# Kernel optimization log

Measured on AMD Instinct MI355X. Metric: run time of the kernel, lower is better.

The kernel has to match this reference:

```python
import jax, jax.numpy as jnp
import numpy as np

B, P, N, E = 4, 4, 4096, 512
QKV_DIM, HEADS = 512, 8
DH = QKV_DIM // HEADS
EPS = 1e-12  # F.normalize default eps


def setup_inputs() -> dict:
    key = jax.random.key(0)
    ks = jax.random.split(key, 5)
    s = 1.0 / np.sqrt(E)
    return {
        "x": jax.random.normal(ks[0], (B, P, N, E), dtype=jnp.float32),
        "w_qkv": jax.random.normal(ks[1], (3 * QKV_DIM, E), dtype=jnp.float32) * s,
        "b_qkv": jax.random.normal(ks[2], (3 * QKV_DIM,), dtype=jnp.float32) * 0.01,
        "temperature": jnp.ones((HEADS, 1, 1), dtype=jnp.float32),
        "w_out": jax.random.normal(ks[3], (E, QKV_DIM), dtype=jnp.float32) * (1.0 / np.sqrt(QKV_DIM)),
        "b_out": jax.random.normal(ks[4], (E,), dtype=jnp.float32) * 0.01,
    }


def _l2norm(t):
    # F.normalize(t, dim=-1): t / max(||t||_2, eps)
    n = jnp.sqrt(jnp.sum(t * t, axis=-1, keepdims=True))
    return t / jnp.maximum(n, EPS)


def reference(x, w_qkv, b_qkv, temperature, w_out, b_out):
    b, p, n, _ = x.shape
    qkv = x @ w_qkv.T + b_qkv                      # (b,p,n,3*qkv)
    q, k, v = jnp.split(qkv, 3, axis=-1)
    def to_heads(t):
        # (b,p,n,h*dh) -> (b,p,h,dh,n)  (channels-as-tokens)
        t = t.reshape(b, p, n, HEADS, DH)
        return jnp.transpose(t, (0, 1, 3, 4, 2))
    q, k, v = to_heads(q), to_heads(k), to_heads(v)
    q = _l2norm(q)                                  # normalize over tokens n
    k = _l2norm(k)
    # channel-wise (dh x dh) attention per head, temperature-scaled
    attn = jnp.einsum('bphdn,bphen->bphde', q, k) * temperature  # (b,p,h,dh,dh)
    attn = jax.nn.softmax(attn, axis=-1)
    out = jnp.einsum('bphde,bphen->bphdn', attn, v)               # (b,p,h,dh,n)
    # torch rearrange 'b p h n d -> b p d (h n)' on (b,p,h,dh,n) -> (b,p,n,h*dh)
    out = jnp.transpose(out, (0, 1, 4, 2, 3)).reshape(b, p, n, HEADS * DH)
    return out @ w_out.T + b_out
```

## Files before the change

kernel.cpp:

```cpp
#include <hip/hip_runtime.h>
#include <stdint.h>

typedef unsigned short u16;
typedef __bf16 bf16x8 __attribute__((ext_vector_type(8)));
typedef float f32x4 __attribute__((ext_vector_type(4)));

#define AS1 __attribute__((address_space(1)))
#define AS3 __attribute__((address_space(3)))

__device__ __forceinline__ void gload_lds16(u16* lds_wave_base, const u16* g) {
  __builtin_amdgcn_global_load_lds((AS1 void*)g, (AS3 void*)lds_wave_base, 16, 0, 0);
}

__device__ __forceinline__ u16 f2bf(float f) {
  unsigned int u = __float_as_uint(f);
  u += 0x7fffu + ((u >> 16) & 1u);
  return (u16)(u >> 16);
}

__global__ void cast_f32_bf16(const float* __restrict__ in, u16* __restrict__ out, int n8) {
  int i = blockIdx.x * blockDim.x + threadIdx.x;
  if (i >= n8) return;
  const float4* p = (const float4*)in + (size_t)i * 2;
  float4 a = p[0], b = p[1];
  uint2 lo, hi;
  lo.x = (unsigned)f2bf(a.x) | ((unsigned)f2bf(a.y) << 16);
  lo.y = (unsigned)f2bf(a.z) | ((unsigned)f2bf(a.w) << 16);
  hi.x = (unsigned)f2bf(b.x) | ((unsigned)f2bf(b.y) << 16);
  hi.y = (unsigned)f2bf(b.z) | ((unsigned)f2bf(b.w) << 16);
  uint2* o = (uint2*)out + (size_t)i * 2;
  o[0] = lo;
  o[1] = hi;
}

template <int MODE>
__global__ __launch_bounds__(256) void gemm_bt(const u16* __restrict__ gA,
                                               const u16* __restrict__ gB,
                                               const float* __restrict__ bias,
                                               void* __restrict__ gC) {
  __shared__ __align__(16) u16 As[128 * 32];
  __shared__ __align__(16) u16 Bs[128 * 32];
  const int t = threadIdx.x;
  const int w = t >> 6, l = t & 63;
  const int lrow = l & 15, quad = l >> 4;
  const int wm = (w >> 1) * 64, wn = (w & 1) * 64;
  const int m0 = blockIdx.x * 128, n0 = blockIdx.y * 128;
  if (MODE == 2) {
    gA += (size_t)blockIdx.z * (512 * 512);
    gB += (size_t)blockIdx.z * (4096 * 512);
  }
  const int srow = w * 32 + (l >> 2);
  const int scol = (l & 3) * 8;
  const u16* ga0 = gA + (size_t)(m0 + srow) * 512 + scol;
  const u16* ga1 = gA + (size_t)(m0 + srow + 16) * 512 + scol;
  const u16* gb0 = gB + (size_t)(n0 + srow) * 512 + scol;
  const u16* gb1 = gB + (size_t)(n0 + srow + 16) * 512 + scol;
  u16* lA0 = &As[w * 1024];
  u16* lA1 = &As[w * 1024 + 512];
  u16* lB0 = &Bs[w * 1024];
  u16* lB1 = &Bs[w * 1024 + 512];

  f32x4 acc[4][4];
#pragma unroll
  for (int mi = 0; mi < 4; ++mi)
#pragma unroll
    for (int ni = 0; ni < 4; ++ni) acc[mi][ni] = (f32x4){0.f, 0.f, 0.f, 0.f};

#pragma unroll 1
  for (int k0 = 0; k0 < 512; k0 += 32) {
    gload_lds16(lA0, ga0 + k0);
    gload_lds16(lA1, ga1 + k0);
    gload_lds16(lB0, gb0 + k0);
    gload_lds16(lB1, gb1 + k0);
    __syncthreads();
    bf16x8 af[4], bfr[4];
#pragma unroll
    for (int mi = 0; mi < 4; ++mi)
      af[mi] = *(const bf16x8*)&As[(wm + mi * 16 + lrow) * 32 + quad * 8];
#pragma unroll
    for (int ni = 0; ni < 4; ++ni)
      bfr[ni] = *(const bf16x8*)&Bs[(wn + ni * 16 + lrow) * 32 + quad * 8];
#pragma unroll
    for (int mi = 0; mi < 4; ++mi)
#pragma unroll
      for (int ni = 0; ni < 4; ++ni)
        acc[mi][ni] = __builtin_amdgcn_mfma_f32_16x16x32_bf16(af[mi], bfr[ni], acc[mi][ni], 0, 0, 0);
    __syncthreads();
  }

#pragma unroll
  for (int mi = 0; mi < 4; ++mi) {
    const int mrow = m0 + wm + mi * 16 + quad * 4;
#pragma unroll
    for (int ni = 0; ni < 4; ++ni) {
      const int ncol = n0 + wn + ni * 16 + lrow;
      f32x4 v = acc[mi][ni];
      if (MODE == 0) {
        const int bp = mrow >> 12, n = mrow & 4095;
        const float bb = bias[ncol];
        uint2 pk;
        pk.x = (unsigned)f2bf(v[0] + bb) | ((unsigned)f2bf(v[1] + bb) << 16);
        pk.y = (unsigned)f2bf(v[2] + bb) | ((unsigned)f2bf(v[3] + bb) << 16);
        *(uint2*)((u16*)gC + (((size_t)bp << 22) + ((size_t)ncol << 12) + n)) = pk;
      } else if (MODE == 1) {
        const int bp = ncol >> 12, n = ncol & 4095;
        const float4 bb = *(const float4*)&bias[1024 + mrow];
        uint2 pk;
        pk.x = (unsigned)f2bf(v[0] + bb.x) | ((unsigned)f2bf(v[1] + bb.y) << 16);
        pk.y = (unsigned)f2bf(v[2] + bb.z) | ((unsigned)f2bf(v[3] + bb.w) << 16);
        *(uint2*)((u16*)gC + ((size_t)bp * (4096 * 512) + (size_t)n * 512 + mrow)) = pk;
      } else {
        const float4 bb = *(const float4*)&bias[mrow];
        float4 o;
        o.x = v[0] + bb.x;
        o.y = v[1] + bb.y;
        o.z = v[2] + bb.z;
        o.w = v[3] + bb.w;
        *(float4*)((float*)gC + (((size_t)blockIdx.z * 4096 + ncol) * 512 + mrow)) = o;
      }
    }
  }
}

__global__ __launch_bounds__(512) void attn_weff(const u16* __restrict__ QKt,
                                                 const u16* __restrict__ wout,
                                                 const float* __restrict__ temperature,
                                                 u16* __restrict__ Weff) {
  __shared__ __align__(16) float sattn[64 * 64];
  __shared__ __align__(16) u16 sattnT[64 * 64];
  __shared__ float rn[128];
  const int blk = blockIdx.x;
  const int bp = blk >> 3, h = blk & 7;
  const int t = threadIdx.x, w = t >> 6, l = t & 63;
  const int lrow = l & 15, quad = l >> 4;
  const u16* base = QKt + ((size_t)bp << 22);

  for (int i = t; i < 4096; i += 512) sattn[i] = 0.f;

#pragma unroll 1
  for (int rr = 0; rr < 16; ++rr) {
    const int i = w * 16 + rr;
    const int ch = (i < 64) ? (h * 64 + i) : (448 + h * 64 + i);
    const u16* row = base + ((size_t)ch << 12);
    float s = 0.f;
#pragma unroll
    for (int it = 0; it < 8; ++it) {
      bf16x8 a = *(const bf16x8*)(row + (it * 64 + l) * 8);
#pragma unroll
      for (int j = 0; j < 8; ++j) {
        float vv = (float)a[j];
        s += vv * vv;
      }
    }
#pragma unroll
    for (int off = 1; off < 64; off <<= 1) s += __shfl_xor(s, off);
    if (l == 0) rn[i] = 1.f / fmaxf(sqrtf(s), 1e-12f);
  }

  f32x4 acc[4][4];
#pragma unroll
  for (int mi = 0; mi < 4; ++mi)
#pragma unroll
    for (int ni = 0; ni < 4; ++ni) acc[mi][ni] = (f32x4){0.f, 0.f, 0.f, 0.f};
  const u16* qb = base + ((size_t)(h * 64) << 12);
  const u16* kb = base + ((size_t)(512 + h * 64) << 12);
  const int nbase = w * 512;
#pragma unroll 1
  for (int ks = 0; ks < 16; ++ks) {
    const int nn = nbase + ks * 32 + quad * 8;
    bf16x8 af[4], bfr[4];
#pragma unroll
    for (int mi = 0; mi < 4; ++mi)
      af[mi] = *(const bf16x8*)(qb + (((size_t)(mi * 16 + lrow)) << 12) + nn);
#pragma unroll
    for (int ni = 0; ni < 4; ++ni)
      bfr[ni] = *(const bf16x8*)(kb + (((size_t)(ni * 16 + lrow)) << 12) + nn);
#pragma unroll
    for (int mi = 0; mi < 4; ++mi)
#pragma unroll
      for (int ni = 0; ni < 4; ++ni)
        acc[mi][ni] = __builtin_amdgcn_mfma_f32_16x16x32_bf16(af[mi], bfr[ni], acc[mi][ni], 0, 0, 0);
  }
  __syncthreads();
  for (int ww = 0; ww < 8; ++ww) {
    if (w == ww) {
#pragma unroll
      for (int mi = 0; mi < 4; ++mi)
#pragma unroll
        for (int ni = 0; ni < 4; ++ni)
#pragma unroll
          for (int r = 0; r < 4; ++r)
            sattn[(mi * 16 + quad * 4 + r) * 64 + ni * 16 + lrow] += acc[mi][ni][r];
    }
    __syncthreads();
  }

  if (t < 64) {
    const int d = t;
    const float rq = rn[d];
    const float tmp = temperature[h];
    float mx = -1e30f;
    for (int e = 0; e < 64; ++e) {
      const int idx = (e + d) & 63;
      float v = sattn[d * 64 + idx] * rq * rn[64 + idx] * tmp;
      sattn[d * 64 + idx] = v;
      mx = fmaxf(mx, v);
    }
    float s = 0.f;
    for (int e = 0; e < 64; ++e) {
      const int idx = (e + d) & 63;
      float p = __expf(sattn[d * 64 + idx] - mx);
      s += p;
      sattn[d * 64 + idx] = p;
    }
    const float inv = 1.f / s;
    for (int e = 0; e < 64; ++e) sattnT[e * 64 + d] = f2bf(sattn[d * 64 + e] * inv);
  }
  __syncthreads();

  bf16x8 a0[4], a1[4];
#pragma unroll
  for (int mi = 0; mi < 4; ++mi) {
    a0[mi] = *(const bf16x8*)&sattnT[(mi * 16 + lrow) * 64 + quad * 8];
    a1[mi] = *(const bf16x8*)&sattnT[(mi * 16 + lrow) * 64 + 32 + quad * 8];
  }
  u16* wb = Weff + ((size_t)bp * (512 * 512));
#pragma unroll 1
  for (int nb = 0; nb < 4; ++nb) {
    const int co = (w * 4 + nb) * 16 + lrow;
    const u16* wrow = wout + (size_t)co * 512 + h * 64;
    bf16x8 b0 = *(const bf16x8*)(wrow + quad * 8);
    bf16x8 b1 = *(const bf16x8*)(wrow + 32 + quad * 8);
#pragma unroll
    for (int mi = 0; mi < 4; ++mi) {
      f32x4 c = (f32x4){0.f, 0.f, 0.f, 0.f};
      c = __builtin_amdgcn_mfma_f32_16x16x32_bf16(a0[mi], b0, c, 0, 0, 0);
      c = __builtin_amdgcn_mfma_f32_16x16x32_bf16(a1[mi], b1, c, 0, 0, 0);
      const int e0 = mi * 16 + quad * 4;
      uint2 pk;
      pk.x = (unsigned)f2bf(c[0]) | ((unsigned)f2bf(c[1]) << 16);
      pk.y = (unsigned)f2bf(c[2]) | ((unsigned)f2bf(c[3]) << 16);
      *(uint2*)(wb + (size_t)co * 512 + h * 64 + e0) = pk;
    }
  }
}

extern "C" void kernel_launch(void* const* d_in, const int* in_sizes, int n_in,
                              void* d_out, int out_size, void* d_ws, size_t ws_size,
                              hipStream_t stream) {
  const float* x      = (const float*)d_in[0];
  const float* w_qkv  = (const float*)d_in[1];
  const float* b_qkv  = (const float*)d_in[2];
  const float* temp   = (const float*)d_in[3];
  const float* w_out  = (const float*)d_in[4];
  const float* b_out  = (const float*)d_in[5];
  float* y = (float*)d_out;

  char* ws = (char*)d_ws;
  u16* x_bf    = (u16*)(ws);
  u16* wqkv_bf = (u16*)(ws + 67108864);
  u16* wout_bf = (u16*)(ws + 68681728);
  u16* QKt     = (u16*)(ws + 69206016);
  u16* V_nat   = (u16*)(ws + 203423744);
  u16* Weff    = (u16*)(ws + 270532608);

  cast_f32_bf16<<<16384, 256, 0, stream>>>(x, x_bf, 33554432 / 8);
  cast_f32_bf16<<<384, 256, 0, stream>>>(w_qkv, wqkv_bf, 786432 / 8);
  cast_f32_bf16<<<128, 256, 0, stream>>>(w_out, wout_bf, 262144 / 8);

  gemm_bt<0><<<dim3(512, 8), 256, 0, stream>>>(x_bf, wqkv_bf, b_qkv, QKt);
  gemm_bt<1><<<dim3(4, 512), 256, 0, stream>>>(wqkv_bf + 1024 * 512, x_bf, b_qkv, V_nat);
  attn_weff<<<128, 512, 0, stream>>>(QKt, wout_bf, temp, Weff);
  gemm_bt<2><<<dim3(4, 32, 16), 256, 0, stream>>>(Weff, V_nat, b_out, y);
}
```

Baseline: 591.0 us.

## Stage GEMM epilogue through LDS and fuse Q/K norm sums into QKV GEMM

The MODE 0/1 GEMM epilogues now transpose the output tile through padded LDS and write coalesced 16-byte rows, replacing the scattered 8-byte stores. The QKV GEMM also accumulates per-channel sums of squares and adds them into a workspace buffer with atomics, so attn_weff no longer rereads the whole Q/K tensor to compute L2 norms. Grid order for MODE 0 is swapped so adjacent blocks walk along tokens. This adds a memset, float atomics whose order is nondeterministic, and norms taken from fp32 values rather than the rounded bf16 ones.

```diff
diff --git a/kernel.cpp b/kernel.cpp
--- a/kernel.cpp
+++ b/kernel.cpp
@@ -37,24 +37,30 @@
 __global__ __launch_bounds__(256) void gemm_bt(const u16* __restrict__ gA,
                                                const u16* __restrict__ gB,
                                                const float* __restrict__ bias,
-                                               void* __restrict__ gC) {
-  __shared__ __align__(16) u16 As[128 * 32];
-  __shared__ __align__(16) u16 Bs[128 * 32];
+                                               void* __restrict__ gC,
+                                               float* __restrict__ ssq) {
+  constexpr int SMEM_U16 = (MODE == 2) ? 8192 : (128 * 136);
+  __shared__ __align__(16) u16 smem[SMEM_U16];
+  u16* As = smem;
+  u16* Bs = smem + 4096;
   const int t = threadIdx.x;
   const int w = t >> 6, l = t & 63;
   const int lrow = l & 15, quad = l >> 4;
   const int wm = (w >> 1) * 64, wn = (w & 1) * 64;
-  const int m0 = blockIdx.x * 128, n0 = blockIdx.y * 128;
+  const int m0 = (MODE == 0 ? blockIdx.y : blockIdx.x) * 128;
+  const int n0 = (MODE == 0 ? blockIdx.x : blockIdx.y) * 128;
+  const u16* pA = gA;
+  const u16* pB = gB;
   if (MODE == 2) {
-    gA += (size_t)blockIdx.z * (512 * 512);
-    gB += (size_t)blockIdx.z * (4096 * 512);
+    pA += (size_t)blockIdx.z * (512 * 512);
+    pB += (size_t)blockIdx.z * (4096 * 512);
   }
   const int srow = w * 32 + (l >> 2);
   const int scol = (l & 3) * 8;
-  const u16* ga0 = gA + (size_t)(m0 + srow) * 512 + scol;
-  const u16* ga1 = gA + (size_t)(m0 + srow + 16) * 512 + scol;
-  const u16* gb0 = gB + (size_t)(n0 + srow) * 512 + scol;
-  const u16* gb1 = gB + (size_t)(n0 + srow + 16) * 512 + scol;
+  const u16* ga0 = pA + (size_t)(m0 + srow) * 512 + scol;
+  const u16* ga1 = pA + (size_t)(m0 + srow + 16) * 512 + scol;
+  const u16* gb0 = pB + (size_t)(n0 + srow) * 512 + scol;
+  const u16* gb1 = pB + (size_t)(n0 + srow + 16) * 512 + scol;
   u16* lA0 = &As[w * 1024];
   u16* lA1 = &As[w * 1024 + 512];
   u16* lB0 = &Bs[w * 1024];
@@ -88,29 +94,15 @@
     __syncthreads();
   }
 
-#pragma unroll
-  for (int mi = 0; mi < 4; ++mi) {
-    const int mrow = m0 + wm + mi * 16 + quad * 4;
-#pragma unroll
-    for (int ni = 0; ni < 4; ++ni) {
-      const int ncol = n0 + wn + ni * 16 + lrow;
-      f32x4 v = acc[mi][ni];
-      if (MODE == 0) {
-        const int bp = mrow >> 12, n = mrow & 4095;
-        const float bb = bias[ncol];
-        uint2 pk;
-        pk.x = (unsigned)f2bf(v[0] + bb) | ((unsigned)f2bf(v[1] + bb) << 16);
-        pk.y = (unsigned)f2bf(v[2] + bb) | ((unsigned)f2bf(v[3] + bb) << 16);
-        *(uint2*)((u16*)gC + (((size_t)bp << 22) + ((size_t)ncol << 12) + n)) = pk;
-      } else if (MODE == 1) {
-        const int bp = ncol >> 12, n = ncol & 4095;
-        const float4 bb = *(const float4*)&bias[1024 + mrow];
-        uint2 pk;
-        pk.x = (unsigned)f2bf(v[0] + bb.x) | ((unsigned)f2bf(v[1] + bb.y) << 16);
-        pk.y = (unsigned)f2bf(v[2] + bb.z) | ((unsigned)f2bf(v[3] + bb.w) << 16);
-        *(uint2*)((u16*)gC + ((size_t)bp * (4096 * 512) + (size_t)n * 512 + mrow)) = pk;
-      } else {
-        const float4 bb = *(const float4*)&bias[mrow];
+  if (MODE == 2) {
+#pragma unroll
+    for (int mi = 0; mi < 4; ++mi) {
+      const int mrow = m0 + wm + mi * 16 + quad * 4;
+      const float4 bb = *(const float4*)&bias[mrow];
+#pragma unroll
+      for (int ni = 0; ni < 4; ++ni) {
+        const int ncol = n0 + wn + ni * 16 + lrow;
+        f32x4 v = acc[mi][ni];
         float4 o;
         o.x = v[0] + bb.x;
         o.y = v[1] + bb.y;
@@ -119,12 +111,70 @@
         *(float4*)((float*)gC + (((size_t)blockIdx.z * 4096 + ncol) * 512 + mrow)) = o;
       }
     }
+  } else {
+    float ss[4] = {0.f, 0.f, 0.f, 0.f};
+#pragma unroll
+    for (int mi = 0; mi < 4; ++mi) {
+      const int mrow_l = wm + mi * 16 + quad * 4;
+#pragma unroll
+      for (int ni = 0; ni < 4; ++ni) {
+        const int ncol_l = wn + ni * 16 + lrow;
+        f32x4 v = acc[mi][ni];
+        float f0, f1, f2, f3;
+        if (MODE == 0) {
+          const float bb = bias[n0 + ncol_l];
+          f0 = v[0] + bb;
+          f1 = v[1] + bb;
+          f2 = v[2] + bb;
+          f3 = v[3] + bb;
+          ss[ni] += f0 * f0 + f1 * f1 + f2 * f2 + f3 * f3;
+        } else {
+          const float4 bb = *(const float4*)&bias[1024 + m0 + mrow_l];
+          f0 = v[0] + bb.x;
+          f1 = v[1] + bb.y;
+          f2 = v[2] + bb.z;
+          f3 = v[3] + bb.w;
+        }
+        uint2 pk;
+        pk.x = (unsigned)f2bf(f0) | ((unsigned)f2bf(f1) << 16);
+        pk.y = (unsigned)f2bf(f2) | ((unsigned)f2bf(f3) << 16);
+        *(uint2*)&smem[ncol_l * 136 + mrow_l] = pk;
+      }
+    }
+    if (MODE == 0) {
+#pragma unroll
+      for (int ni = 0; ni < 4; ++ni) {
+        float s = ss[ni];
+        s += __shfl_xor(s, 16);
+        s += __shfl_xor(s, 32);
+        if (quad == 0)
+          atomicAdd(&ssq[((m0 >> 12) << 10) + n0 + wn + ni * 16 + lrow], s);
+      }
+    }
+    __syncthreads();
+    u16* outp = (u16*)gC;
+#pragma unroll
+    for (int j = 0; j < 8; ++j) {
+      const int g = j * 256 + t;
+      const int r = g >> 4;
+      const int c = (g & 15) * 8;
+      uint4 val = *(const uint4*)&smem[r * 136 + c];
+      size_t gaddr;
+      if (MODE == 0) {
+        gaddr = ((size_t)(m0 >> 12) << 22) + ((size_t)(n0 + r) << 12) + (size_t)((m0 & 4095) + c);
+      } else {
+        const int tokg = n0 + r;
+        gaddr = (size_t)(tokg >> 12) * (4096 * 512) + (size_t)(tokg & 4095) * 512 + (size_t)(m0 + c);
+      }
+      *(uint4*)(outp + gaddr) = val;
+    }
   }
 }
 
 __global__ __launch_bounds__(512) void attn_weff(const u16* __restrict__ QKt,
                                                  const u16* __restrict__ wout,
                                                  const float* __restrict__ temperature,
+                                                 const float* __restrict__ ssq,
                                                  u16* __restrict__ Weff) {
   __shared__ __align__(16) float sattn[64 * 64];
   __shared__ __align__(16) u16 sattnT[64 * 64];
@@ -137,24 +187,10 @@
 
   for (int i = t; i < 4096; i += 512) sattn[i] = 0.f;
 
-#pragma unroll 1
-  for (int rr = 0; rr < 16; ++rr) {
-    const int i = w * 16 + rr;
-    const int ch = (i < 64) ? (h * 64 + i) : (448 + h * 64 + i);
-    const u16* row = base + ((size_t)ch << 12);
-    float s = 0.f;
-#pragma unroll
-    for (int it = 0; it < 8; ++it) {
-      bf16x8 a = *(const bf16x8*)(row + (it * 64 + l) * 8);
-#pragma unroll
-      for (int j = 0; j < 8; ++j) {
-        float vv = (float)a[j];
-        s += vv * vv;
-      }
-    }
-#pragma unroll
-    for (int off = 1; off < 64; off <<= 1) s += __shfl_xor(s, off);
-    if (l == 0) rn[i] = 1.f / fmaxf(sqrtf(s), 1e-12f);
+  if (t < 128) {
+    const int ch = (t < 64) ? (h * 64 + t) : (448 + h * 64 + t);
+    const float nn = sqrtf(ssq[(bp << 10) + ch]);
+    rn[t] = 1.f / fmaxf(nn, 1e-12f);
   }
 
   f32x4 acc[4][4];
@@ -263,13 +299,15 @@
   u16* QKt     = (u16*)(ws + 69206016);
   u16* V_nat   = (u16*)(ws + 203423744);
   u16* Weff    = (u16*)(ws + 270532608);
-
+  float* ssq   = (float*)(ws + 278921216);
+
+  hipMemsetAsync(ssq, 0, 16 * 1024 * sizeof(float), stream);
   cast_f32_bf16<<<16384, 256, 0, stream>>>(x, x_bf, 33554432 / 8);
   cast_f32_bf16<<<384, 256, 0, stream>>>(w_qkv, wqkv_bf, 786432 / 8);
   cast_f32_bf16<<<128, 256, 0, stream>>>(w_out, wout_bf, 262144 / 8);
 
-  gemm_bt<0><<<dim3(512, 8), 256, 0, stream>>>(x_bf, wqkv_bf, b_qkv, QKt);
-  gemm_bt<1><<<dim3(4, 512), 256, 0, stream>>>(wqkv_bf + 1024 * 512, x_bf, b_qkv, V_nat);
-  attn_weff<<<128, 512, 0, stream>>>(QKt, wout_bf, temp, Weff);
-  gemm_bt<2><<<dim3(4, 32, 16), 256, 0, stream>>>(Weff, V_nat, b_out, y);
-}
+  gemm_bt<0><<<dim3(8, 512), 256, 0, stream>>>(x_bf, wqkv_bf, b_qkv, QKt, ssq);
+  gemm_bt<1><<<dim3(4, 512), 256, 0, stream>>>(wqkv_bf + 1024 * 512, x_bf, b_qkv, V_nat, nullptr);
+  attn_weff<<<128, 512, 0, stream>>>(QKt, wout_bf, temp, ssq, Weff);
+  gemm_bt<2><<<dim3(4, 32, 16), 256, 0, stream>>>(Weff, V_nat, b_out, y, nullptr);
+}
```

New measurement: 542.8 us. 8.2% less time.
